# Kernel tuning notes

Hardware: AMD Instinct MI355X
Metric: run time of the kernel (lower is better)

The kernel has to match this reference:

```python
import jax, jax.numpy as jnp
import numpy as np

L = 2
S = (L + 1) ** 2            # 9 spherical harmonic coefficients
C = 128                     # sphere_channels
H = 128                     # hidden_channels
NH = 8                      # num_heads
A = 32                      # attn_alpha_channels
V = 16                      # attn_value_channels
N = 5000                    # nodes
E = 50000                   # edges
DE = 128                    # invariant edge embedding dim
G = 18                      # S2 grid points

# l of each coefficient in l-major layout [S]
L_OF = np.concatenate([np.full(2 * l + 1, l) for l in range(L + 1)])
IDX_M0 = np.array([l * l + l for l in range(L + 1)])

def _idx_m(m):
    neg = np.array([l * l + l - m for l in range(m, L + 1)])
    pos = np.array([l * l + l + m for l in range(m, L + 1)])
    return neg, pos

IDX_M1_NEG, IDX_M1_POS = _idx_m(1)
IDX_M2_NEG, IDX_M2_POS = _idx_m(2)
# m-major ordering and its inverse permutation back to l-major
PERM = np.concatenate([IDX_M0, IDX_M1_POS, IDX_M1_NEG, IDX_M2_POS, IDX_M2_NEG])
INV_PERM = np.argsort(PERM)


def _silu(x):
    return x * jax.nn.sigmoid(x)


def _layernorm(x, g, b, eps=1e-5):
    mu = x.mean(-1, keepdims=True)
    var = ((x - mu) ** 2).mean(-1, keepdims=True)
    return (x - mu) * jax.lax.rsqrt(var + eps) * g + b


def _smooth_leaky_relu(x, a=0.2):
    return 0.5 * (1 + a) * x + 0.5 * (1 - a) * x * (2 * jax.nn.sigmoid(x) - 1)


def _so2_conv(x, w_m0, b_m0, w_m1, w_m2, cout):
    """SO(2) convolution on rotated embeddings. x: [E,S,Cin] l-major.
    Returns ([E,S,cout] l-major, extra m=0 channels)."""
    e = x.shape[0]
    # m = 0: plain linear over flattened (L+1)*Cin
    x0 = x[:, IDX_M0, :].reshape(e, -1)
    y0 = x0 @ w_m0 + b_m0
    y0_main = y0[:, : (L + 1) * cout].reshape(e, L + 1, cout)
    y0_extra = y0[:, (L + 1) * cout:]
    parts = [y0_main]
    # m > 0: complex (cos/sin) SO2 mixing with shared weight for real/imag
    for neg, pos, w in ((IDX_M1_NEG, IDX_M1_POS, w_m1), (IDX_M2_NEG, IDX_M2_POS, w_m2)):
        nl = len(neg)
        xr = x[:, pos, :].reshape(e, -1)
        xi = x[:, neg, :].reshape(e, -1)
        yr = xr @ w  # [E, 2*nl*cout]
        yi = xi @ w
        yr_r, yr_i = yr[:, : nl * cout], yr[:, nl * cout:]
        yi_r, yi_i = yi[:, : nl * cout], yi[:, nl * cout:]
        parts.append((yr_r - yi_i).reshape(e, nl, cout))   # +m (real)
        parts.append((yr_i + yi_r).reshape(e, nl, cout))   # -m (imag)
    out_m = jnp.concatenate(parts, axis=1)                 # m-major
    return out_m[:, INV_PERM, :], y0_extra


def _s2_act(x, togrid, fromgrid):
    g = jnp.einsum('gs,esc->egc', togrid, x)
    return jnp.einsum('sg,egc->esc', fromgrid, _silu(g))


def _sep_s2_act(scalars, x, togrid, fromgrid):
    t = _s2_act(x, togrid, fromgrid)
    return jnp.concatenate([_silu(scalars)[:, None, :], t[:, 1:, :]], axis=1)


def _so3_linear(x, w, b):
    # w: [L+1, Cin, Cout], shared across m within each l; bias only on l=0
    out = jnp.einsum('nsc,sco->nso', x, w[L_OF])
    return out.at[:, 0, :].add(b)


def _eqv_norm(x, g, b, eps=1e-5):
    # l=0: layernorm over channels; l>0: RMS over (m, channels) per degree
    outs = [_layernorm(x[:, 0:1, :], g[0], b)]
    for l in range(1, L + 1):
        sl = x[:, l * l:(l + 1) * (l + 1), :]
        rms = jnp.sqrt(jnp.mean(sl ** 2, axis=(1, 2), keepdims=True) + eps)
        outs.append(sl / rms * g[l])
    return jnp.concatenate(outs, axis=1)


def _forward(x, edge_distance, wigner, rad_w1, rad_b1, rad_ln_g, rad_ln_b, rad_w2, rad_b2,
             w1_m0, b1_m0, w1_m1, w1_m2, w2_m0, b2_m0, w2_m1, w2_m2,
             alpha_ln_g, alpha_ln_b, alpha_dot, proj_w, proj_b,
             norm1_g, norm1_b, norm2_g, norm2_b,
             gate_w, gate_b, ffn_w1, ffn_b1, ffn_w2, ffn_b2,
             togrid, fromgrid, edge_src, edge_dst):
    # ---------- SO2 equivariant graph attention ----------
    xn = _eqv_norm(x, norm1_g, norm1_b)
    msg = jnp.concatenate([xn[edge_src], xn[edge_dst]], axis=-1)      # [E,S,2C]
    msg = jnp.einsum('eij,ejc->eic', wigner, msg)                     # rotate to edge frame
    # radial function shared across m within each l (use_m_share_rad)
    h = _silu(_layernorm(edge_distance @ rad_w1 + rad_b1, rad_ln_g, rad_ln_b))
    rad = (h @ rad_w2 + rad_b2).reshape(-1, L + 1, 2 * C)             # [E,L+1,2C]
    msg = msg * rad[:, L_OF, :]
    hid, x0_extra = _so2_conv(msg, w1_m0, b1_m0, w1_m1, w1_m2, H)
    x_alpha = x0_extra[:, : NH * A].reshape(-1, NH, A)
    gating = x0_extra[:, NH * A:]                                     # [E,H]
    hid = _sep_s2_act(gating, hid, togrid, fromgrid)
    val, _ = _so2_conv(hid, w2_m0, b2_m0, w2_m1, w2_m2, NH * V)
    val = jnp.einsum('eji,ejc->eic', wigner, val)                     # rotate back (D^T)
    # attention weights with per-destination segment softmax
    a = _smooth_leaky_relu(_layernorm(x_alpha, alpha_ln_g, alpha_ln_b))
    a = jnp.einsum('eha,ha->eh', a, alpha_dot)                        # [E,NH]
    amax = jax.ops.segment_max(a, edge_dst, num_segments=N)
    aexp = jnp.exp(a - amax[edge_dst])
    asum = jax.ops.segment_sum(aexp, edge_dst, num_segments=N)
    attn = aexp / asum[edge_dst]
    msg_out = (val.reshape(-1, S, NH, V) * attn[:, None, :, None]).reshape(-1, S, NH * V)
    node = jax.ops.segment_sum(msg_out, edge_dst, num_segments=N)     # [N,S,NH*V]
    x = x + _so3_linear(node, proj_w, proj_b)
    # ---------- spherical FFN (sep S2 gating) ----------
    xn = _eqv_norm(x, norm2_g, norm2_b)
    gating = xn[:, 0, :] @ gate_w + gate_b
    hh = _so3_linear(xn, ffn_w1, ffn_b1)
    hh = _sep_s2_act(gating, hh, togrid, fromgrid)
    return x + _so3_linear(hh, ffn_w2, ffn_b2)


def setup_inputs() -> dict:
    key = jax.random.key(0)
    ks = iter(jax.random.split(key, 64))
    def nrm(shape, scale=1.0):
        return jax.random.normal(next(ks), shape, dtype=jnp.float32) * scale
    EX = NH * A + H
    inp = {}
    inp['x'] = nrm((N, S, C))
    inp['edge_distance'] = nrm((E, DE))
    inp['wigner'] = nrm((E, S, S), 1.0 / np.sqrt(S))
    inp['rad_w1'] = nrm((DE, 64), 1.0 / np.sqrt(DE)); inp['rad_b1'] = jnp.zeros((64,), jnp.float32)
    inp['rad_ln_g'] = jnp.ones((64,), jnp.float32); inp['rad_ln_b'] = jnp.zeros((64,), jnp.float32)
    inp['rad_w2'] = nrm((64, 2 * C * (L + 1)), 0.05); inp['rad_b2'] = jnp.ones((2 * C * (L + 1),), jnp.float32)
    inp['w1_m0'] = nrm(((L + 1) * 2 * C, (L + 1) * H + EX), 1.0 / np.sqrt((L + 1) * 2 * C))
    inp['b1_m0'] = jnp.zeros(((L + 1) * H + EX,), jnp.float32)
    inp['w1_m1'] = nrm((2 * 2 * C, 2 * 2 * H), 1.0 / np.sqrt(2 * 2 * C))
    inp['w1_m2'] = nrm((2 * C, 2 * H), 1.0 / np.sqrt(2 * C))
    inp['w2_m0'] = nrm(((L + 1) * H, (L + 1) * NH * V), 1.0 / np.sqrt((L + 1) * H))
    inp['b2_m0'] = jnp.zeros(((L + 1) * NH * V,), jnp.float32)
    inp['w2_m1'] = nrm((2 * H, 2 * 2 * NH * V), 1.0 / np.sqrt(2 * H))
    inp['w2_m2'] = nrm((H, 2 * NH * V), 1.0 / np.sqrt(H))
    inp['alpha_ln_g'] = jnp.ones((A,), jnp.float32); inp['alpha_ln_b'] = jnp.zeros((A,), jnp.float32)
    inp['alpha_dot'] = nrm((NH, A), 1.0 / np.sqrt(A))
    inp['proj_w'] = nrm((L + 1, NH * V, C), 1.0 / np.sqrt(NH * V)); inp['proj_b'] = jnp.zeros((C,), jnp.float32)
    inp['norm1_g'] = jnp.ones((L + 1, C), jnp.float32); inp['norm1_b'] = jnp.zeros((C,), jnp.float32)
    inp['norm2_g'] = jnp.ones((L + 1, C), jnp.float32); inp['norm2_b'] = jnp.zeros((C,), jnp.float32)
    inp['gate_w'] = nrm((C, H), 1.0 / np.sqrt(C)); inp['gate_b'] = jnp.zeros((H,), jnp.float32)
    inp['ffn_w1'] = nrm((L + 1, C, H), 1.0 / np.sqrt(C)); inp['ffn_b1'] = jnp.zeros((H,), jnp.float32)
    inp['ffn_w2'] = nrm((L + 1, H, C), 1.0 / np.sqrt(H)); inp['ffn_b2'] = jnp.zeros((C,), jnp.float32)
    inp['togrid'] = nrm((G, S), 1.0 / np.sqrt(S))
    inp['fromgrid'] = nrm((S, G), 1.0 / np.sqrt(G))
    inp['edge_src'] = jax.random.randint(next(ks), (E,), 0, N)
    inp['edge_dst'] = jax.random.randint(next(ks), (E,), 0, N)
    return inp


def reference(x, edge_distance, wigner, rad_w1, rad_b1, rad_ln_g, rad_ln_b, rad_w2, rad_b2,
              w1_m0, b1_m0, w1_m1, w1_m2, w2_m0, b2_m0, w2_m1, w2_m2,
              alpha_ln_g, alpha_ln_b, alpha_dot, proj_w, proj_b,
              norm1_g, norm1_b, norm2_g, norm2_b,
              gate_w, gate_b, ffn_w1, ffn_b1, ffn_w2, ffn_b2,
              togrid, fromgrid, edge_src, edge_dst):
    return _forward(x, edge_distance, wigner, rad_w1, rad_b1, rad_ln_g, rad_ln_b, rad_w2, rad_b2,
                    w1_m0, b1_m0, w1_m1, w1_m2, w2_m0, b2_m0, w2_m1, w2_m2,
                    alpha_ln_g, alpha_ln_b, alpha_dot, proj_w, proj_b,
                    norm1_g, norm1_b, norm2_g, norm2_b,
                    gate_w, gate_b, ffn_w1, ffn_b1, ffn_w2, ffn_b2,
                    togrid, fromgrid, edge_src, edge_dst)
```

## Files before the change

### kernel.cpp

```cpp
#include <hip/hip_runtime.h>
#include <hip/hip_bf16.h>

typedef unsigned short u16;
typedef unsigned int   u32;
typedef __attribute__((ext_vector_type(8))) short short8;
typedef __attribute__((ext_vector_type(4))) float float4v;

#define NN 5000
#define EE 50000

__device__ __forceinline__ float b2f(u16 u){ return __uint_as_float(((u32)u)<<16); }
__device__ __forceinline__ u16 f2b(float f){
  u32 x = __float_as_uint(f);
  u32 r = (x + 0x7fffu + ((x>>16)&1u)) >> 16;
  return (u16)r;
}
__device__ __forceinline__ float ldin(const void* p, size_t i, bool f32){
  return f32 ? ((const float*)p)[i] : b2f(((const u16*)p)[i]);
}
__device__ __forceinline__ float siluf(float x){ return x/(1.f+__expf(-x)); }
__device__ __forceinline__ float waveRedSum(float v){
  #pragma unroll
  for (int m=32;m>=1;m>>=1) v += __shfl_xor(v,m,64);
  return v;
}
__device__ __forceinline__ float red32(float v){
  #pragma unroll
  for (int m=16;m>=1;m>>=1) v += __shfl_xor(v,m,64);
  return v;
}
__device__ __forceinline__ void gload_lds16(const u16* g, u16* l){
  __builtin_amdgcn_global_load_lds((const __attribute__((address_space(1))) void*)g,
                                   (__attribute__((address_space(3))) void*)l, 16, 0, 0);
}


__global__ __launch_bounds__(256) void zero_kernel(float* __restrict__ p, int n){
  for (int i = blockIdx.x*256 + threadIdx.x; i < n; i += gridDim.x*256) p[i] = 0.f;
}

__global__ void detect_kernel(const u32* __restrict__ ng, int* __restrict__ flag){
  if (blockIdx.x == 0 && threadIdx.x == 0) *flag = (ng[0] == 0x3F800000u) ? 1 : 0;
}

__global__ __launch_bounds__(256) void hist_kernel(const int* __restrict__ edst,
    int* __restrict__ counts){
  int e = blockIdx.x*256 + threadIdx.x;
  if (e < EE) atomicAdd(&counts[edst[e]], 1);
}

__global__ __launch_bounds__(1024) void scan_kernel(const int* __restrict__ counts,
    int* __restrict__ row_start, int* __restrict__ cursor){
  __shared__ int buf[1024];
  __shared__ int base;
  const int t = threadIdx.x;
  if (t == 0){ base = 0; row_start[0] = 0; }
  __syncthreads();
  for (int i0 = 0; i0 < NN; i0 += 1024){
    int i = i0 + t;
    int c = (i < NN) ? counts[i] : 0;
    buf[t] = c;
    __syncthreads();
    #pragma unroll
    for (int ofs = 1; ofs < 1024; ofs <<= 1){
      int v = (t >= ofs) ? buf[t-ofs] : 0;
      __syncthreads();
      buf[t] += v;
      __syncthreads();
    }
    if (i < NN){
      int incl = base + buf[t];
      row_start[i+1] = incl;
      cursor[i] = incl - c;
    }
    __syncthreads();
    if (t == 0) base += buf[1023];
    __syncthreads();
  }
}

__global__ __launch_bounds__(256) void place_kernel(const int* __restrict__ edst,
    int* __restrict__ cursor, int* __restrict__ order){
  int e = blockIdx.x*256 + threadIdx.x;
  if (e < EE) order[atomicAdd(&cursor[edst[e]], 1)] = e;
}

__global__ __launch_bounds__(256) void gathercvt_kernel(const int* __restrict__ dflag,
    const void* __restrict__ src, const int* __restrict__ order, int e0,
    u16* __restrict__ dst, int n){
  const bool f32 = (*dflag != 0);
  for (int i = blockIdx.x*256 + threadIdx.x; i < n; i += gridDim.x*256){
    int le = i >> 7, c = i & 127;
    int eg = order[e0 + le];
    dst[i] = f2b(ldin(src, (size_t)eg*128 + c, f32));
  }
}

__device__ __forceinline__ void do_cvtT(bool f32, const void* src, u16* dst,
    int K, int N, int tid, int stride){
  int total = K*N;
  for (int i = tid; i < total; i += stride){
    int n = i / K, k = i - n*K;
    dst[i] = f2b(ldin(src, (size_t)k*N + n, f32));
  }
}
__device__ __forceinline__ void do_cvtT3(bool f32, const void* src, u16* dst,
    int tid, int stride){
  for (int i = tid; i < 49152; i += stride){
    int l = i >> 14, j = i & 16383;
    int n = j >> 7, k = j & 127;
    dst[i] = f2b(ldin(src, (size_t)l*16384 + (size_t)k*128 + n, f32));
  }
}
__device__ __forceinline__ void do_wprepT(bool f32, const void* w, u16* wt,
    int K0, int N0, int tid, int stride){
  int total = 4*N0*K0;
  for (int i = tid; i < total; i += stride){
    int c = i / (2*K0), rr0 = i - c*2*K0;
    float v;
    if (rr0 < K0) v = ldin(w, (size_t)rr0*2*N0 + c, f32);
    else {
      int rr = rr0 - K0;
      if (c < N0) v = -ldin(w, (size_t)rr*2*N0 + N0 + c, f32);
      else        v =  ldin(w, (size_t)rr*2*N0 + (c - N0), f32);
    }
    wt[i] = f2b(v);
  }
}

__global__ __launch_bounds__(256) void prep_all_kernel(const int* __restrict__ dflag,
    const void* w1_m0, const void* w2_m0, const void* rad_w1, const void* rad_w2,
    const void* proj_w, const void* ffn_w1, const void* ffn_w2, const void* gate_w,
    const void* b1, const void* b2, const void* rb1, const void* rb2,
    const void* pb, const void* gb, const void* f1, const void* f2,
    const void* w1_m1, const void* w1_m2, const void* w2_m1, const void* w2_m2,
    const void* togrid, const void* fromgrid,
    u16* w1m0T, u16* w2m0T, u16* rw1T, u16* rw2T,
    u16* projT3, u16* ffn1T3, u16* ffn2T3, u16* gateT,
    u16* b1m0C, u16* b2m0C, u16* rb1C, u16* rb2C,
    u16* pbC, u16* gbC, u16* fb1C, u16* fb2C,
    u16* W1cT, u16* W2cT, u16* W3cT, u16* W4cT,
    float* TGf, float* FGf){
  const bool f32 = (*dflag != 0);
  const int tid = blockIdx.x*256 + threadIdx.x;
  const int stride = gridDim.x*256;
  switch (blockIdx.y){
    case 0:  do_cvtT (f32, w1_m0, w1m0T, 768, 768, tid, stride); break;
    case 1:  do_cvtT (f32, w2_m0, w2m0T, 384, 384, tid, stride); break;
    case 2:  do_cvtT (f32, rad_w1, rw1T, 128, 64,  tid, stride); break;
    case 3:  do_cvtT (f32, rad_w2, rw2T, 64, 768,  tid, stride); break;
    case 4:  do_cvtT3(f32, proj_w, projT3, tid, stride); break;
    case 5:  do_cvtT3(f32, ffn_w1, ffn1T3, tid, stride); break;
    case 6:  do_cvtT3(f32, ffn_w2, ffn2T3, tid, stride); break;
    case 7:  do_cvtT (f32, gate_w, gateT, 128, 128, tid, stride); break;
    case 8:
      if (tid < 768) b1m0C[tid] = f2b(ldin(b1, tid, f32));
      if (tid < 384) b2m0C[tid] = f2b(ldin(b2, tid, f32));
      if (tid < 64)  rb1C[tid]  = f2b(ldin(rb1, tid, f32));
      if (tid < 768) rb2C[tid]  = f2b(ldin(rb2, tid, f32));
      if (tid < 128){
        pbC[tid]  = f2b(ldin(pb, tid, f32));
        gbC[tid]  = f2b(ldin(gb, tid, f32));
        fb1C[tid] = f2b(ldin(f1, tid, f32));
        fb2C[tid] = f2b(ldin(f2, tid, f32));
      }
      break;
    case 9:  do_wprepT(f32, w1_m1, W1cT, 512, 256, tid, stride); break;
    case 10: do_wprepT(f32, w1_m2, W2cT, 256, 128, tid, stride); break;
    case 11: do_wprepT(f32, w2_m1, W3cT, 256, 256, tid, stride); break;
    case 12: do_wprepT(f32, w2_m2, W4cT, 128, 128, tid, stride); break;
    case 13:
      if (tid < 162) TGf[tid] = ldin(togrid, tid, f32);
      else if (tid >= 256 && tid < 418) FGf[tid-256] = ldin(fromgrid, tid-256, f32);
      break;
  }
}

__global__ __launch_bounds__(128) void eqvnorm_kernel(const int* __restrict__ dflag,
    const void* __restrict__ x, int in_always_f32,
    const void* __restrict__ g, const void* __restrict__ b,
    void* __restrict__ out, int out_f32){
  const bool f32 = (*dflag != 0);
  const bool inf32 = in_always_f32 || f32;
  const int n = blockIdx.x, t = threadIdx.x;
  __shared__ float red[2];
  float v[9];
  #pragma unroll
  for (int s=0;s<9;s++) v[s] = ldin(x, (size_t)n*1152 + s*128 + t, inf32);

  auto bsum = [&](float val)->float{
    float w = waveRedSum(val);
    __syncthreads();
    if ((t & 63) == 0) red[t>>6] = w;
    __syncthreads();
    return red[0] + red[1];
  };
  auto store = [&](int idx, float val){
    if (out_f32) ((float*)out)[(size_t)n*1152 + idx] = val;
    else         ((u16*) out)[(size_t)n*1152 + idx] = f2b(val);
  };
  float mu  = bsum(v[0]) * (1.f/128.f);
  float d0  = v[0] - mu;
  float var = bsum(d0*d0) * (1.f/128.f);
  store(t, d0 * rsqrtf(var + 1e-5f) * ldin(g, t, f32) + ldin(b, t, f32));
  float ss1 = v[1]*v[1] + v[2]*v[2] + v[3]*v[3];
  float inv1 = rsqrtf(bsum(ss1)*(1.f/384.f) + 1e-5f);
  float g1 = ldin(g, 128 + t, f32);
  #pragma unroll
  for (int s=1;s<=3;s++) store(s*128 + t, v[s]*inv1*g1);
  float ss2 = 0.f;
  #pragma unroll
  for (int s=4;s<9;s++) ss2 += v[s]*v[s];
  float inv2 = rsqrtf(bsum(ss2)*(1.f/640.f) + 1e-5f);
  float g2 = ldin(g, 256 + t, f32);
  #pragma unroll
  for (int s=4;s<9;s++) store(s*128 + t, v[s]*inv2*g2);
}

__device__ __forceinline__ void gemm_core(u16* AsB, u16* BsB,
    const u16* __restrict__ A, int lda, int K,
    const u16* __restrict__ Wt, int NOUT,
    const u16* __restrict__ bias,
    u16* __restrict__ out0, int ld0, int coloff0, int split,
    u16* __restrict__ out1, int ld1, int M, int r0, int n0){
  const int t = threadIdx.x;
  const int lane = t & 63, wave = t >> 6;
  const int wr = (wave & 1) * 64, wn = (wave >> 1) * 64;
  float4v acc[4][4];
  #pragma unroll
  for (int i=0;i<4;i++)
    #pragma unroll
    for (int j=0;j<4;j++) acc[i][j] = (float4v){0.f,0.f,0.f,0.f};

  const int fr = lane & 15;
  const int fq = (((lane >> 4) ^ ((fr >> 1) & 3)) * 8);

  const int Rw   = wave * 32;
  const int srow = lane >> 2;
  const int scol = (((lane & 3) ^ ((srow >> 1) & 3)) * 8);
  const u16* aG0 = A  + (size_t)(r0 + Rw + srow) * lda + scol;
  const u16* aG1 = aG0 + (size_t)16 * lda;
  const bool aV0 = (r0 + Rw + srow)      < M;
  const bool aV1 = (r0 + Rw + 16 + srow) < M;
  const u16* bG0 = Wt + (size_t)(n0 + Rw + srow) * K + scol;
  const u16* bG1 = bG0 + (size_t)16 * K;
  const bool bV0 = (n0 + Rw + srow)      < NOUT;
  const bool bV1 = (n0 + Rw + 16 + srow) < NOUT;

  auto stage = [&](int buf, int k0){
    u16* lA = AsB + buf*4096 + Rw * 32;
    u16* lB = BsB + buf*4096 + Rw * 32;
    if (aV0) gload_lds16(aG0 + k0, lA);
    if (aV1) gload_lds16(aG1 + k0, lA + 16*32);
    if (bV0) gload_lds16(bG0 + k0, lB);
    if (bV1) gload_lds16(bG1 + k0, lB + 16*32);
  };

  stage(0, 0);
  __syncthreads();
  int cur = 0;
  for (int k0 = 0; k0 < K; k0 += 32){
    const int k1 = k0 + 32;
    if (k1 < K) stage(cur ^ 1, k1);
    short8 af[4], bfv[4];
    #pragma unroll
    for (int i=0;i<4;i++){
      af[i]  = *(const short8*)&AsB[cur*4096 + (wr + i*16 + fr)*32 + fq];
      bfv[i] = *(const short8*)&BsB[cur*4096 + (wn + i*16 + fr)*32 + fq];
    }
    #pragma unroll
    for (int i=0;i<4;i++)
      #pragma unroll
      for (int j=0;j<4;j++)
        acc[i][j] = __builtin_amdgcn_mfma_f32_16x16x32_bf16(af[i], bfv[j], acc[i][j], 0, 0, 0);
    __syncthreads();
    cur ^= 1;
  }
  const int quad = lane >> 4;
  #pragma unroll
  for (int j=0;j<4;j++){
    int col = n0 + wn + j*16 + fr;
    if (col >= NOUT) continue;
    float bv = bias ? b2f(bias[col]) : 0.f;
    #pragma unroll
    for (int i=0;i<4;i++){
      int rbase = r0 + wr + i*16 + quad*4;
      #pragma unroll
      for (int rg=0; rg<4; rg++){
        int row = rbase + rg;
        if (row >= M) continue;
        float v = acc[i][j][rg] + bv;
        if (col < split) out0[(size_t)row*ld0 + coloff0 + col] = f2b(v);
        else             out1[(size_t)row*ld1 + (col - split)] = f2b(v);
      }
    }
  }
}

__device__ __forceinline__ int xcd_swz(int bid, int nwg){
  const int q = nwg >> 3, r = nwg & 7;
  const int xcd = bid & 7, sid = bid >> 3;
  return (xcd < r ? xcd*(q+1) : r*(q+1) + (xcd - r)*q) + sid;
}

__global__ __launch_bounds__(256) void gemm_mfma_kernel(
    const u16* __restrict__ A, int lda, int K,
    const u16* __restrict__ Wt, int NOUT,
    const u16* __restrict__ bias,
    u16* __restrict__ out0, int ld0, int coloff0, int split,
    u16* __restrict__ out1, int ld1, int M){
  __shared__ __align__(16) u16 As[2][128*32];
  __shared__ __align__(16) u16 Bs[2][128*32];
  const int nxg = gridDim.x, nyg = gridDim.y;
  const int bid = blockIdx.y * nxg + blockIdx.x;
  const int swz = xcd_swz(bid, nxg*nyg);
  const int mt = swz / nyg;
  gemm_core(&As[0][0], &Bs[0][0], A, lda, K, Wt, NOUT, bias,
            out0, ld0, coloff0, split, out1, ld1, M, mt*128, (swz - mt*nyg)*128);
}

struct GemmJob {
  const u16* A; const u16* Wt; const u16* bias; u16* out0; u16* out1;
  int lda, K, NOUT, ld0, coloff0, split, ld1;
};
__global__ __launch_bounds__(256) void gemm_mfma3_kernel(
    GemmJob j0, GemmJob j1, GemmJob j2, int ny0, int ny01, int M){
  __shared__ __align__(16) u16 As[2][128*32];
  __shared__ __align__(16) u16 Bs[2][128*32];
  const int nxg = gridDim.x, nyg = gridDim.y;
  const int bid = blockIdx.y * nxg + blockIdx.x;
  const int swz = xcd_swz(bid, nxg*nyg);
  const int mt = swz / nyg;
  const int y  = swz - mt*nyg;
  GemmJob j; int yt;
  if (y < ny0)       { j = j0; yt = y; }
  else if (y < ny01) { j = j1; yt = y - ny0; }
  else               { j = j2; yt = y - ny01; }
  gemm_core(&As[0][0], &Bs[0][0], j.A, j.lda, j.K, j.Wt, j.NOUT, j.bias,
            j.out0, j.ld0, j.coloff0, j.split, j.out1, j.ld1, M, mt*128, yt*128);
}

__global__ __launch_bounds__(256) void gemm_node_kernel(
    const int* __restrict__ dflag,
    const u16* __restrict__ A,
    const u16* __restrict__ W3t,
    const u16* __restrict__ bias,
    const void* __restrict__ resid, int resid_mode,
    void* __restrict__ out, int out_mode, int gate_out){
  const bool f32 = (*dflag != 0);
  const int l = blockIdx.y;
  const int rpn  = (l==0) ? 1 : ((l==1) ? 3 : 5);
  const int soff = (l==0) ? 0 : ((l==1) ? 1 : 4);
  const int M = NN * rpn;
  const int r0 = blockIdx.x * 128;
  if (r0 >= M) return;
  __shared__ __align__(16) u16 As[128][40];
  __shared__ __align__(16) u16 Bs[128][40];
  const int t = threadIdx.x;
  const int lane = t & 63, wave = t >> 6;
  const int wr = (wave & 1) * 64, wn = (wave >> 1) * 64;
  float4v acc[4][4];
  #pragma unroll
  for (int i=0;i<4;i++)
    #pragma unroll
    for (int j=0;j<4;j++) acc[i][j] = (float4v){0.f,0.f,0.f,0.f};

  const int sr = t >> 2, sc = (t & 3) * 8;
  const int fr = lane & 15, fq = (lane >> 4) * 8;
  size_t abase[2]; bool aval[2];
  #pragma unroll
  for (int s2=0;s2<2;s2++){
    int m = r0 + sr + s2*64;
    aval[s2] = m < M;
    int n = m / rpn, srow = soff + (m % rpn);
    abase[s2] = (size_t)n*1152 + srow*128 + sc;
  }
  const u16* Wl = W3t + (size_t)l*16384;

  #pragma unroll
  for (int k0 = 0; k0 < 128; k0 += 32){
    #pragma unroll
    for (int s2=0;s2<2;s2++){
      int row = sr + s2*64;
      uint4 av = make_uint4(0u,0u,0u,0u);
      if (aval[s2]) av = *(const uint4*)(A + abase[s2] + k0);
      *(uint4*)&As[row][sc] = av;
      uint4 wv = *(const uint4*)(Wl + (size_t)row*128 + k0 + sc);
      *(uint4*)&Bs[row][sc] = wv;
    }
    __syncthreads();
    short8 af[4], bfr[4];
    #pragma unroll
    for (int i=0;i<4;i++){
      af[i]  = *(const short8*)&As[wr + i*16 + fr][fq];
      bfr[i] = *(const short8*)&Bs[wn + i*16 + fr][fq];
    }
    #pragma unroll
    for (int i=0;i<4;i++)
      #pragma unroll
      for (int j=0;j<4;j++)
        acc[i][j] = __builtin_amdgcn_mfma_f32_16x16x32_bf16(af[i], bfr[j], acc[i][j], 0, 0, 0);
    __syncthreads();
  }
  const int quad = lane >> 4;
  #pragma unroll
  for (int j=0;j<4;j++){
    int col = wn + j*16 + fr;
    float bv = (bias && l==0) ? b2f(bias[col]) : 0.f;
    #pragma unroll
    for (int i=0;i<4;i++){
      int rbase = r0 + wr + i*16 + quad*4;
      #pragma unroll
      for (int rg=0; rg<4; rg++){
        int m = rbase + rg;
        if (m >= M) continue;
        int n = m / rpn, srow = soff + (m % rpn);
        size_t na = (size_t)n*1152 + srow*128 + col;
        float v = acc[i][j][rg] + bv;
        if (resid_mode == 1)      v += ((const float*)resid)[na];
        else if (resid_mode == 2) v += ldin(resid, na, f32);
        if (gate_out)            ((u16*)out)[(size_t)n*128 + col] = f2b(v);
        else if (out_mode == 0)  ((u16*)out)[na] = f2b(v);
        else if (out_mode == 1)  ((float*)out)[na] = v;
        else { if (f32) ((float*)out)[na] = v; else ((u16*)out)[na] = f2b(v); }
      }
    }
  }
}

__global__ __launch_bounds__(256) void nodecvt_kernel(const float* __restrict__ node,
    const float* __restrict__ nsum, u16* __restrict__ nodeb){
  for (int i = blockIdx.x*256 + threadIdx.x; i < NN*1152; i += gridDim.x*256){
    int n = i / 1152, c = i & 127, h = c >> 4;
    float ns = nsum[(size_t)n*8 + h];
    float rs = (ns > 0.f) ? 1.f/ns : 0.f;
    nodeb[i] = f2b(node[i] * rs);
  }
}

__global__ __launch_bounds__(128) void node_s2act_kernel(
    const u16* __restrict__ hh, const u16* __restrict__ gating,
    const float* __restrict__ TGf, const float* __restrict__ FGf, u16* __restrict__ hh2){
  const int n = blockIdx.x, t = threadIdx.x;
  float hv[9];
  #pragma unroll
  for (int s=0;s<9;s++) hv[s] = b2f(hh[(size_t)n*1152 + s*128 + t]);
  float gg[18];
  #pragma unroll
  for (int gi=0;gi<18;gi++) gg[gi] = 0.f;
  #pragma unroll
  for (int s=0;s<9;s++){
    float hvs = hv[s];
    #pragma unroll
    for (int gi=0;gi<18;gi++) gg[gi] = fmaf(TGf[gi*9+s], hvs, gg[gi]);
  }
  #pragma unroll
  for (int gi=0;gi<18;gi++) gg[gi] = siluf(gg[gi]);
  hh2[(size_t)n*1152 + t] = f2b(siluf(b2f(gating[(size_t)n*128 + t])));
  #pragma unroll
  for (int s=1;s<9;s++){
    float a = 0.f;
    #pragma unroll
    for (int gi=0;gi<18;gi++) a = fmaf(FGf[s*18+gi], gg[gi], a);
    hh2[(size_t)n*1152 + s*128 + t] = f2b(a);
  }
}

__global__ __launch_bounds__(256) void lnsilu_kernel(const int* __restrict__ dflag,
    u16* __restrict__ H, const void* __restrict__ rlng, const void* __restrict__ rlnb, int M){
  const bool f32 = (*dflag != 0);
  const int r = blockIdx.x*4 + (threadIdx.x >> 6), lane = threadIdx.x & 63;
  if (r >= M) return;
  float h = b2f(H[(size_t)r*64 + lane]);
  float mu = waveRedSum(h) * (1.f/64.f);
  float d = h - mu;
  float var = waveRedSum(d*d) * (1.f/64.f);
  float hn = d * rsqrtf(var + 1e-5f) * ldin(rlng, lane, f32) + ldin(rlnb, lane, f32);
  H[(size_t)r*64 + lane] = f2b(siluf(hn));
}

__global__ __launch_bounds__(256) void edge_rot_kernel(const int* __restrict__ dflag,
    const u16* __restrict__ xn, const void* __restrict__ wig,
    const u16* __restrict__ rad,
    const int* __restrict__ esrc, const int* __restrict__ edst,
    const int* __restrict__ order, int e0, u16* __restrict__ msg){
  const bool f32 = (*dflag != 0);
  const int le = blockIdx.x, t = threadIdx.x;
  const int eg = order[e0 + le];
  __shared__ float W[81];
  if (t < 81) W[t] = ldin(wig, (size_t)eg*81 + t, f32);
  const int src = esrc[eg], dst = edst[eg];
  float pre[9];
  const u16* base = (t < 128) ? (xn + (size_t)src*1152 + t) : (xn + (size_t)dst*1152 + (t-128));
  #pragma unroll
  for (int j=0;j<9;j++) pre[j] = b2f(base[j*128]);
  __syncthreads();
  float rot[9];
  #pragma unroll
  for (int i=0;i<9;i++){
    float a = 0.f;
    #pragma unroll
    for (int j=0;j<9;j++) a = fmaf(W[i*9+j], pre[j], a);
    rot[i] = a;
  }
  float r[3];
  #pragma unroll
  for (int l=0;l<3;l++) r[l] = b2f(rad[(size_t)le*768 + l*256 + t]);
  const int INVP[9] = {0,5,1,3,8,6,2,4,7};
  const int LOF[9]  = {0,1,1,1,2,2,2,2,2};
  u16* mb = msg + (size_t)le*2304 + t;
  #pragma unroll
  for (int i=0;i<9;i++) mb[INVP[i]*256] = f2b(rot[i] * r[LOF[i]]);
}

__global__ __launch_bounds__(256) void s2act_alpha_kernel(const int* __restrict__ dflag,
    const u16* __restrict__ hid, const u16* __restrict__ extra,
    const float* __restrict__ TGf, const float* __restrict__ FGf,
    const void* __restrict__ alng, const void* __restrict__ alnb, const void* __restrict__ adot,
    const int* __restrict__ edst, const int* __restrict__ order, int e0,
    u16* __restrict__ hid2, float* __restrict__ aexp, float* __restrict__ nsum){
  const bool f32 = (*dflag != 0);
  const int le = blockIdx.x, t = threadIdx.x;
  const int p = e0 + le;
  {
    const int h = t >> 5, ai = t & 31;
    float v = b2f(extra[(size_t)le*384 + t]);
    float mu = red32(v) * (1.f/32.f);
    float d = v - mu;
    float var = red32(d*d) * (1.f/32.f);
    float xh = d * rsqrtf(var + 1e-5f) * ldin(alng, ai, f32) + ldin(alnb, ai, f32);
    float sig = 1.f/(1.f + __expf(-xh));
    float sl = 0.6f*xh + 0.4f*xh*(2.f*sig - 1.f);
    float pp = sl * ldin(adot, h*32 + ai, f32);
    float dot = red32(pp);
    if (ai == 0){
      float ex = __expf(dot - 8.f);
      aexp[(size_t)p*8 + h] = ex;
      atomicAdd(&nsum[(size_t)edst[order[p]]*8 + h], ex);
    }
  }
  if (t < 128){
    const int INVP[9] = {0,5,1,3,8,6,2,4,7};
    float hv[9];
    #pragma unroll
    for (int s=0;s<9;s++) hv[s] = b2f(hid[(size_t)le*1152 + INVP[s]*128 + t]);
    float gg[18];
    #pragma unroll
    for (int gi=0;gi<18;gi++) gg[gi] = 0.f;
    #pragma unroll
    for (int s=0;s<9;s++){
      float hvs = hv[s];
      #pragma unroll
      for (int gi=0;gi<18;gi++) gg[gi] = fmaf(TGf[gi*9+s], hvs, gg[gi]);
    }
    #pragma unroll
    for (int gi=0;gi<18;gi++) gg[gi] = siluf(gg[gi]);
    hid2[(size_t)le*1152 + t] = f2b(siluf(b2f(extra[(size_t)le*384 + 256 + t])));
    #pragma unroll
    for (int s=1;s<9;s++){
      float a = 0.f;
      #pragma unroll
      for (int gi=0;gi<18;gi++) a = fmaf(FGf[s*18+gi], gg[gi], a);
      hid2[(size_t)le*1152 + INVP[s]*128 + t] = f2b(a);
    }
  }
}

__global__ __launch_bounds__(128) void unrot_gather_kernel(const int* __restrict__ dflag,
    const u16* __restrict__ val, const void* __restrict__ wig,
    const float* __restrict__ aexp, const int* __restrict__ order,
    const int* __restrict__ row_start, int e0, int Mc, float* __restrict__ node){
  const bool f32 = (*dflag != 0);
  const int n = blockIdx.x, t = threadIdx.x;
  const int s = row_start[n], tend = row_start[n+1];
  int lo = (s > e0) ? s : e0;
  int hi = (tend < e0 + Mc) ? tend : (e0 + Mc);
  if (lo >= hi) return;
  __shared__ float W[81];
  __shared__ float SC[8];
  const int INVP[9] = {0,5,1,3,8,6,2,4,7};
  float acc[9];
  #pragma unroll
  for (int i=0;i<9;i++) acc[i] = 0.f;
  for (int p = lo; p < hi; p++){
    const int le = p - e0;
    const int eg = order[p];
    __syncthreads();
    if (t < 81) W[t] = ldin(wig, (size_t)eg*81 + t, f32);
    if (t >= 120) SC[t-120] = aexp[(size_t)p*8 + (t-120)];
    __syncthreads();
    float vs[9];
    #pragma unroll
    for (int j=0;j<9;j++) vs[j] = b2f(val[(size_t)le*1152 + INVP[j]*128 + t]);
    const float sc = SC[t>>4];
    #pragma unroll
    for (int i=0;i<9;i++){
      float a = 0.f;
      #pragma unroll
      for (int j=0;j<9;j++) a = fmaf(W[j*9+i], vs[j], a);
      acc[i] = fmaf(a, sc, acc[i]);
    }
  }
  const bool full = (s >= e0) && (tend <= e0 + Mc);
  #pragma unroll
  for (int i=0;i<9;i++){
    float* dst = &node[(size_t)n*1152 + i*128 + t];
    if (full) *dst = acc[i];
    else      atomicAdd(dst, acc[i]);
  }
}

extern "C" void kernel_launch(void* const* d_in, const int* in_sizes, int n_in,
                              void* d_out, int out_size, void* d_ws, size_t ws_size,
                              hipStream_t stream){
  (void)in_sizes; (void)n_in; (void)out_size;
  const void* x       = d_in[0];
  const void* edist   = d_in[1];
  const void* wig     = d_in[2];
  const void* rad_w1  = d_in[3];
  const void* rad_b1  = d_in[4];
  const void* rad_lng = d_in[5];
  const void* rad_lnb = d_in[6];
  const void* rad_w2  = d_in[7];
  const void* rad_b2  = d_in[8];
  const void* w1_m0   = d_in[9];
  const void* b1_m0   = d_in[10];
  const void* w1_m1   = d_in[11];
  const void* w1_m2   = d_in[12];
  const void* w2_m0   = d_in[13];
  const void* b2_m0   = d_in[14];
  const void* w2_m1   = d_in[15];
  const void* w2_m2   = d_in[16];
  const void* alng    = d_in[17];
  const void* alnb    = d_in[18];
  const void* adot    = d_in[19];
  const void* proj_w  = d_in[20];
  const void* proj_b  = d_in[21];
  const void* norm1_g = d_in[22];
  const void* norm1_b = d_in[23];
  const void* norm2_g = d_in[24];
  const void* norm2_b = d_in[25];
  const void* gate_w  = d_in[26];
  const void* gate_b  = d_in[27];
  const void* ffn_w1  = d_in[28];
  const void* ffn_b1  = d_in[29];
  const void* ffn_w2  = d_in[30];
  const void* ffn_b2  = d_in[31];
  const void* togrid  = d_in[32];
  const void* fromgrid= d_in[33];
  const int* esrc     = (const int*)d_in[34];
  const int* edst     = (const int*)d_in[35];

  char* wsp = (char*)d_ws;
  size_t off = 0;
  auto alloc = [&](size_t bytes)->char*{
    char* p = wsp + off;
    off = (off + bytes + 255) & ~(size_t)255;
    return p;
  };
  int*  dflag  = (int*) alloc(4);
  u16*  W1cT   = (u16*) alloc((size_t)512*1024*2);
  u16*  W2cT   = (u16*) alloc((size_t)256*512*2);
  u16*  W3cT   = (u16*) alloc((size_t)512*512*2);
  u16*  W4cT   = (u16*) alloc((size_t)256*256*2);
  u16*  w1m0T  = (u16*) alloc((size_t)768*768*2);
  u16*  b1m0C  = (u16*) alloc((size_t)768*2);
  u16*  w2m0T  = (u16*) alloc((size_t)384*384*2);
  u16*  b2m0C  = (u16*) alloc((size_t)384*2);
  u16*  rw1T   = (u16*) alloc((size_t)64*128*2);
  u16*  rb1C   = (u16*) alloc((size_t)64*2);
  u16*  rw2T   = (u16*) alloc((size_t)768*64*2);
  u16*  rb2C   = (u16*) alloc((size_t)768*2);
  u16*  projT3 = (u16*) alloc((size_t)3*16384*2);
  u16*  ffn1T3 = (u16*) alloc((size_t)3*16384*2);
  u16*  ffn2T3 = (u16*) alloc((size_t)3*16384*2);
  u16*  gateT  = (u16*) alloc((size_t)16384*2);
  u16*  pbC    = (u16*) alloc((size_t)128*2);
  u16*  gbC    = (u16*) alloc((size_t)128*2);
  u16*  fb1C   = (u16*) alloc((size_t)128*2);
  u16*  fb2C   = (u16*) alloc((size_t)128*2);
  float* TGf   = (float*)alloc((size_t)162*4);
  float* FGf   = (float*)alloc((size_t)162*4);
  u16*  xn     = (u16*) alloc((size_t)NN*1152*2);
  float* aexp  = (float*)alloc((size_t)EE*8*4);
  float* nsum  = (float*)alloc((size_t)NN*8*4);
  float* node  = (float*)alloc((size_t)NN*1152*4);
  int*  counts = (int*) alloc((size_t)NN*4);
  int*  row_st = (int*) alloc((size_t)(NN+1)*4);
  int*  cursor = (int*) alloc((size_t)NN*4);
  int*  order  = (int*) alloc((size_t)EE*4);
  size_t fixed_end = off;
  size_t avail = (ws_size > fixed_end) ? (ws_size - fixed_end) : 0;

  long long cap = ((long long)avail - 4096) / 7680;
  int Ec;
  if (cap >= 50048) Ec = 50048;
  else {
    long long c128 = cap & ~127LL;
    if (c128 < 128) c128 = 128;
    int nch = (EE + (int)c128 - 1) / (int)c128;
    Ec = ((EE + nch - 1) / nch + 127) & ~127;
  }
  char* cb = wsp + fixed_end;
  u16* msgC   = (u16*)cb;
  u16* hidC   = (u16*)(cb + (size_t)Ec*2304*2);
  u16* extraC = (u16*)(cb + (size_t)Ec*2304*2 + (size_t)Ec*1152*2);
  u16* hid2C  = msgC;
  u16* valC   = hidC;
  u16* edistC = msgC;
  u16* radC   = hidC;
  u16* HrawC  = hidC + (size_t)Ec*768;
  u16*  nodeb  = (u16*)cb;
  float* xnew  = (float*)(cb + (size_t)NN*1152*2);
  u16*  xn2    = (u16*)(cb + (size_t)NN*1152*2 + (size_t)NN*1152*4);
  u16*  gating = xn2 + (size_t)NN*1152;
  u16*  hh     = gating + (size_t)NN*128;
  u16*  hh2    = hh + (size_t)NN*1152;

  detect_kernel<<<1, 64, 0, stream>>>((const u32*)norm1_g, dflag);

  zero_kernel<<<2048, 256, 0, stream>>>(nsum, NN*8 + NN*1152 + NN);

  hist_kernel<<<(EE+255)/256, 256, 0, stream>>>(edst, counts);
  scan_kernel<<<1, 1024, 0, stream>>>(counts, row_st, cursor);
  place_kernel<<<(EE+255)/256, 256, 0, stream>>>(edst, cursor, order);

  prep_all_kernel<<<dim3(256,14), 256, 0, stream>>>(dflag,
      w1_m0, w2_m0, rad_w1, rad_w2, proj_w, ffn_w1, ffn_w2, gate_w,
      b1_m0, b2_m0, rad_b1, rad_b2, proj_b, gate_b, ffn_b1, ffn_b2,
      w1_m1, w1_m2, w2_m1, w2_m2, togrid, fromgrid,
      w1m0T, w2m0T, rw1T, rw2T, projT3, ffn1T3, ffn2T3, gateT,
      b1m0C, b2m0C, rb1C, rb2C, pbC, gbC, fb1C, fb2C,
      W1cT, W2cT, W3cT, W4cT, TGf, FGf);

  eqvnorm_kernel<<<NN, 128, 0, stream>>>(dflag, x, 0, norm1_g, norm1_b, xn, 0);

  for (int e0 = 0; e0 < EE; e0 += Ec){
    int Mc = (EE - e0 < Ec) ? (EE - e0) : Ec;
    int GX = (Mc + 127) / 128;
    gathercvt_kernel<<<dim3((Mc*128+255)/256), 256, 0, stream>>>(dflag, edist, order, e0,
                                                                 edistC, Mc*128);
    gemm_mfma_kernel<<<dim3(GX,1), 256, 0, stream>>>(edistC, 128, 128, rw1T, 64, rb1C,
                                                     HrawC, 64, 0, 64, nullptr, 0, Mc);
    lnsilu_kernel<<<dim3((Mc+3)/4), 256, 0, stream>>>(dflag, HrawC, rad_lng, rad_lnb, Mc);
    gemm_mfma_kernel<<<dim3(GX,6), 256, 0, stream>>>(HrawC, 64, 64, rw2T, 768, rb2C,
                                                     radC, 768, 0, 768, nullptr, 0, Mc);
    edge_rot_kernel<<<Mc, 256, 0, stream>>>(dflag, xn, wig, radC, esrc, edst, order, e0, msgC);
    {
      GemmJob j0{msgC,        w1m0T, b1m0C,   hidC, extraC, 2304, 768,  768, 1152, 0,   384, 384};
      GemmJob j1{msgC + 768,  W1cT,  nullptr, hidC, nullptr,2304, 1024, 512, 1152, 384, 512, 0};
      GemmJob j2{msgC + 1792, W2cT,  nullptr, hidC, nullptr,2304, 512,  256, 1152, 896, 256, 0};
      gemm_mfma3_kernel<<<dim3(GX,12), 256, 0, stream>>>(j0, j1, j2, 6, 10, Mc);
    }
    s2act_alpha_kernel<<<Mc, 256, 0, stream>>>(dflag, hidC, extraC, TGf, FGf, alng,
                                               alnb, adot, edst, order, e0, hid2C, aexp, nsum);
    {
      GemmJob j0{hid2C,       w2m0T, b2m0C,   valC, nullptr, 1152, 384, 384, 1152, 0,   384, 0};
      GemmJob j1{hid2C + 384, W3cT,  nullptr, valC, nullptr, 1152, 512, 512, 1152, 384, 512, 0};
      GemmJob j2{hid2C + 896, W4cT,  nullptr, valC, nullptr, 1152, 256, 256, 1152, 896, 256, 0};
      gemm_mfma3_kernel<<<dim3(GX,9), 256, 0, stream>>>(j0, j1, j2, 3, 7, Mc);
    }
    unrot_gather_kernel<<<NN, 128, 0, stream>>>(dflag, valC, wig, aexp, order, row_st,
                                                e0, Mc, node);
  }

  const int GN2 = (NN*5 + 127)/128;
  nodecvt_kernel<<<2048, 256, 0, stream>>>(node, nsum, nodeb);
  gemm_node_kernel<<<dim3(GN2,3), 256, 0, stream>>>(dflag, nodeb, projT3, pbC,
                                                    x, 2, xnew, 1, 0);
  eqvnorm_kernel<<<NN, 128, 0, stream>>>(dflag, xnew, 1, norm2_g, norm2_b, xn2, 0);
  gemm_node_kernel<<<dim3((NN+127)/128,1), 256, 0, stream>>>(dflag, xn2, gateT, gbC,
                                                             nullptr, 0, gating, 0, 1);
  gemm_node_kernel<<<dim3(GN2,3), 256, 0, stream>>>(dflag, xn2, ffn1T3, fb1C,
                                                    nullptr, 0, hh, 0, 0);
  node_s2act_kernel<<<NN, 128, 0, stream>>>(hh, gating, TGf, FGf, hh2);
  gemm_node_kernel<<<dim3(GN2,3), 256, 0, stream>>>(dflag, hh2, ffn2T3, fb2C,
                                                    xnew, 1, d_out, 2, 0);
}
```

Measured before the change: 1.035 ms.

## Pre-convert Wigner matrices to fp32 and read them directly in edge kernels

Adds a prep stage that converts all Wigner matrices into a float32 buffer. The edge rotation and unrotation kernels now read that buffer straight from global memory instead of staging each matrix in shared memory behind barriers. Edge rotation handles two edges per block. The unrotate-gather kernel splits each node's edges across two 128-thread halves and combines their partial sums through shared memory. The aims are fewer syncthreads, more parallelism per node and less per-edge overhead, at the cost of an extra 16 MB fp32 copy and uncached scalar weight loads.

```diff
diff --git a/kernel.cpp b/kernel.cpp
--- a/kernel.cpp
+++ b/kernel.cpp
@@ -134,13 +134,13 @@
     const void* b1, const void* b2, const void* rb1, const void* rb2,
     const void* pb, const void* gb, const void* f1, const void* f2,
     const void* w1_m1, const void* w1_m2, const void* w2_m1, const void* w2_m2,
-    const void* togrid, const void* fromgrid,
+    const void* togrid, const void* fromgrid, const void* wig,
     u16* w1m0T, u16* w2m0T, u16* rw1T, u16* rw2T,
     u16* projT3, u16* ffn1T3, u16* ffn2T3, u16* gateT,
     u16* b1m0C, u16* b2m0C, u16* rb1C, u16* rb2C,
     u16* pbC, u16* gbC, u16* fb1C, u16* fb2C,
     u16* W1cT, u16* W2cT, u16* W3cT, u16* W4cT,
-    float* TGf, float* FGf){
+    float* TGf, float* FGf, float* WIGf){
   const bool f32 = (*dflag != 0);
   const int tid = blockIdx.x*256 + threadIdx.x;
   const int stride = gridDim.x*256;
@@ -173,6 +173,9 @@
       if (tid < 162) TGf[tid] = ldin(togrid, tid, f32);
       else if (tid >= 256 && tid < 418) FGf[tid-256] = ldin(fromgrid, tid-256, f32);
       break;
+    case 14:
+      for (int i = tid; i < EE*81; i += stride) WIGf[i] = ldin(wig, i, f32);
+      break;
   }
 }
 
@@ -479,38 +482,38 @@
   H[(size_t)r*64 + lane] = f2b(siluf(hn));
 }
 
-__global__ __launch_bounds__(256) void edge_rot_kernel(const int* __restrict__ dflag,
-    const u16* __restrict__ xn, const void* __restrict__ wig,
+__global__ __launch_bounds__(256) void edge_rot_kernel(
+    const u16* __restrict__ xn, const float* __restrict__ WIGf,
     const u16* __restrict__ rad,
     const int* __restrict__ esrc, const int* __restrict__ edst,
-    const int* __restrict__ order, int e0, u16* __restrict__ msg){
-  const bool f32 = (*dflag != 0);
-  const int le = blockIdx.x, t = threadIdx.x;
-  const int eg = order[e0 + le];
-  __shared__ float W[81];
-  if (t < 81) W[t] = ldin(wig, (size_t)eg*81 + t, f32);
-  const int src = esrc[eg], dst = edst[eg];
-  float pre[9];
-  const u16* base = (t < 128) ? (xn + (size_t)src*1152 + t) : (xn + (size_t)dst*1152 + (t-128));
-  #pragma unroll
-  for (int j=0;j<9;j++) pre[j] = b2f(base[j*128]);
-  __syncthreads();
-  float rot[9];
-  #pragma unroll
-  for (int i=0;i<9;i++){
-    float a = 0.f;
-    #pragma unroll
-    for (int j=0;j<9;j++) a = fmaf(W[i*9+j], pre[j], a);
-    rot[i] = a;
-  }
-  float r[3];
-  #pragma unroll
-  for (int l=0;l<3;l++) r[l] = b2f(rad[(size_t)le*768 + l*256 + t]);
+    const int* __restrict__ order, int e0, int Mc, u16* __restrict__ msg){
+  const int t = threadIdx.x;
   const int INVP[9] = {0,5,1,3,8,6,2,4,7};
   const int LOF[9]  = {0,1,1,1,2,2,2,2,2};
-  u16* mb = msg + (size_t)le*2304 + t;
-  #pragma unroll
-  for (int i=0;i<9;i++) mb[INVP[i]*256] = f2b(rot[i] * r[LOF[i]]);
+  #pragma unroll
+  for (int e = 0; e < 2; e++){
+    const int le = blockIdx.x*2 + e;
+    if (le >= Mc) return;
+    const int eg = order[e0 + le];
+    const int src = esrc[eg], dst = edst[eg];
+    const float* Wp = WIGf + (size_t)eg*81;
+    const u16* base = (t < 128) ? (xn + (size_t)src*1152 + t)
+                                : (xn + (size_t)dst*1152 + (t-128));
+    float pre[9];
+    #pragma unroll
+    for (int j=0;j<9;j++) pre[j] = b2f(base[j*128]);
+    float r[3];
+    #pragma unroll
+    for (int l=0;l<3;l++) r[l] = b2f(rad[(size_t)le*768 + l*256 + t]);
+    u16* mb = msg + (size_t)le*2304 + t;
+    #pragma unroll
+    for (int i=0;i<9;i++){
+      float a = 0.f;
+      #pragma unroll
+      for (int j=0;j<9;j++) a = fmaf(Wp[i*9+j], pre[j], a);
+      mb[INVP[i]*256] = f2b(a * r[LOF[i]]);
+    }
+  }
 }
 
 __global__ __launch_bounds__(256) void s2act_alpha_kernel(const int* __restrict__ dflag,
@@ -566,47 +569,51 @@
   }
 }
 
-__global__ __launch_bounds__(128) void unrot_gather_kernel(const int* __restrict__ dflag,
-    const u16* __restrict__ val, const void* __restrict__ wig,
+__global__ __launch_bounds__(256) void unrot_gather_kernel(
+    const u16* __restrict__ val, const float* __restrict__ WIGf,
     const float* __restrict__ aexp, const int* __restrict__ order,
     const int* __restrict__ row_start, int e0, int Mc, float* __restrict__ node){
-  const bool f32 = (*dflag != 0);
   const int n = blockIdx.x, t = threadIdx.x;
+  const int g = t >> 7, c = t & 127;
   const int s = row_start[n], tend = row_start[n+1];
   int lo = (s > e0) ? s : e0;
   int hi = (tend < e0 + Mc) ? tend : (e0 + Mc);
   if (lo >= hi) return;
-  __shared__ float W[81];
-  __shared__ float SC[8];
+  __shared__ float partial[9][128];
   const int INVP[9] = {0,5,1,3,8,6,2,4,7};
   float acc[9];
   #pragma unroll
   for (int i=0;i<9;i++) acc[i] = 0.f;
-  for (int p = lo; p < hi; p++){
+  for (int p = lo + g; p < hi; p += 2){
     const int le = p - e0;
     const int eg = order[p];
-    __syncthreads();
-    if (t < 81) W[t] = ldin(wig, (size_t)eg*81 + t, f32);
-    if (t >= 120) SC[t-120] = aexp[(size_t)p*8 + (t-120)];
-    __syncthreads();
+    const float* Wp = WIGf + (size_t)eg*81;
     float vs[9];
     #pragma unroll
-    for (int j=0;j<9;j++) vs[j] = b2f(val[(size_t)le*1152 + INVP[j]*128 + t]);
-    const float sc = SC[t>>4];
+    for (int j=0;j<9;j++) vs[j] = b2f(val[(size_t)le*1152 + INVP[j]*128 + c]);
+    const float sc = aexp[(size_t)p*8 + (c>>4)];
     #pragma unroll
     for (int i=0;i<9;i++){
       float a = 0.f;
       #pragma unroll
-      for (int j=0;j<9;j++) a = fmaf(W[j*9+i], vs[j], a);
+      for (int j=0;j<9;j++) a = fmaf(Wp[j*9+i], vs[j], a);
       acc[i] = fmaf(a, sc, acc[i]);
     }
   }
-  const bool full = (s >= e0) && (tend <= e0 + Mc);
-  #pragma unroll
-  for (int i=0;i<9;i++){
-    float* dst = &node[(size_t)n*1152 + i*128 + t];
-    if (full) *dst = acc[i];
-    else      atomicAdd(dst, acc[i]);
+  if (g == 1){
+    #pragma unroll
+    for (int i=0;i<9;i++) partial[i][c] = acc[i];
+  }
+  __syncthreads();
+  if (g == 0){
+    const bool full = (s >= e0) && (tend <= e0 + Mc);
+    #pragma unroll
+    for (int i=0;i<9;i++){
+      float v = acc[i] + partial[i][c];
+      float* dst = &node[(size_t)n*1152 + i*128 + c];
+      if (full) *dst = v;
+      else      atomicAdd(dst, v);
+    }
   }
 }
 
@@ -681,6 +688,7 @@
   u16*  fb2C   = (u16*) alloc((size_t)128*2);
   float* TGf   = (float*)alloc((size_t)162*4);
   float* FGf   = (float*)alloc((size_t)162*4);
+  float* WIGf  = (float*)alloc((size_t)EE*81*4);
   u16*  xn     = (u16*) alloc((size_t)NN*1152*2);
   float* aexp  = (float*)alloc((size_t)EE*8*4);
   float* nsum  = (float*)alloc((size_t)NN*8*4);
@@ -725,13 +733,13 @@
   scan_kernel<<<1, 1024, 0, stream>>>(counts, row_st, cursor);
   place_kernel<<<(EE+255)/256, 256, 0, stream>>>(edst, cursor, order);
 
-  prep_all_kernel<<<dim3(256,14), 256, 0, stream>>>(dflag,
+  prep_all_kernel<<<dim3(256,15), 256, 0, stream>>>(dflag,
       w1_m0, w2_m0, rad_w1, rad_w2, proj_w, ffn_w1, ffn_w2, gate_w,
       b1_m0, b2_m0, rad_b1, rad_b2, proj_b, gate_b, ffn_b1, ffn_b2,
-      w1_m1, w1_m2, w2_m1, w2_m2, togrid, fromgrid,
+      w1_m1, w1_m2, w2_m1, w2_m2, togrid, fromgrid, wig,
       w1m0T, w2m0T, rw1T, rw2T, projT3, ffn1T3, ffn2T3, gateT,
       b1m0C, b2m0C, rb1C, rb2C, pbC, gbC, fb1C, fb2C,
-      W1cT, W2cT, W3cT, W4cT, TGf, FGf);
+      W1cT, W2cT, W3cT, W4cT, TGf, FGf, WIGf);
 
   eqvnorm_kernel<<<NN, 128, 0, stream>>>(dflag, x, 0, norm1_g, norm1_b, xn, 0);
 
@@ -745,7 +753,8 @@
     lnsilu_kernel<<<dim3((Mc+3)/4), 256, 0, stream>>>(dflag, HrawC, rad_lng, rad_lnb, Mc);
     gemm_mfma_kernel<<<dim3(GX,6), 256, 0, stream>>>(HrawC, 64, 64, rw2T, 768, rb2C,
                                                      radC, 768, 0, 768, nullptr, 0, Mc);
-    edge_rot_kernel<<<Mc, 256, 0, stream>>>(dflag, xn, wig, radC, esrc, edst, order, e0, msgC);
+    edge_rot_kernel<<<dim3((Mc+1)/2), 256, 0, stream>>>(xn, WIGf, radC, esrc, edst,
+                                                        order, e0, Mc, msgC);
     {
       GemmJob j0{msgC,        w1m0T, b1m0C,   hidC, extraC, 2304, 768,  768, 1152, 0,   384, 384};
       GemmJob j1{msgC + 768,  W1cT,  nullptr, hidC, nullptr,2304, 1024, 512, 1152, 384, 512, 0};
@@ -760,7 +769,7 @@
       GemmJob j2{hid2C + 896, W4cT,  nullptr, valC, nullptr, 1152, 256, 256, 1152, 896, 256, 0};
       gemm_mfma3_kernel<<<dim3(GX,9), 256, 0, stream>>>(j0, j1, j2, 3, 7, Mc);
     }
-    unrot_gather_kernel<<<NN, 128, 0, stream>>>(dflag, valC, wig, aexp, order, row_st,
+    unrot_gather_kernel<<<NN, 256, 0, stream>>>(valC, WIGf, aexp, order, row_st,
                                                 e0, Mc, node);
   }
 
```

Result: slower. 1.200 ms (+16.0%).
